# Kernel tuning notes

Measured on AMD Instinct MI355X. Metric: run time of the kernel, lower is better.

The kernel has to match this reference:

```python
import jax, jax.numpy as jnp
import numpy as np

H = 4  # heads


def _tconv(x, src, dst, ea, Wq, bq, Wk, bk, Wv, bv, We, Ws, bs):
    # PyG TransformerConv, heads=4, concat=False, root_weight=True, beta=False
    N = x.shape[0]
    Dh = Wq.shape[1] // H  # per-head dim (= hidden_channels)
    q = (x @ Wq + bq).reshape(N, H, Dh)
    k = (x @ Wk + bk).reshape(N, H, Dh)
    v = (x @ Wv + bv).reshape(N, H, Dh)
    e = (ea @ We).reshape(-1, H, Dh)      # lin_edge has no bias in PyG
    kj = k[src] + e                        # [E, H, Dh]
    vj = v[src] + e                        # [E, H, Dh]
    alpha = (q[dst] * kj).sum(-1) / jnp.sqrt(jnp.asarray(Dh, x.dtype))  # [E, H]
    # segment softmax over incoming edges of each dst node
    m = jax.ops.segment_max(alpha, dst, num_segments=N)
    a = jnp.exp(alpha - m[dst])
    s = jax.ops.segment_sum(a, dst, num_segments=N)
    a = a / (s[dst] + 1e-16)
    out = jax.ops.segment_sum(a[:, :, None] * vj, dst, num_segments=N)  # [N, H, Dh]
    out = out.mean(axis=1)                 # concat=False -> mean over heads
    return out + x @ Ws + bs               # root/skip connection


def setup_inputs() -> dict:
    key = jax.random.key(0)
    ks = jax.random.split(key, 32)
    N, E, C_in, C_e, Ch = 50000, 800000, 32, 16, 32
    d = {}
    d['x'] = jax.random.normal(ks[0], (N, C_in), dtype=jnp.float32)
    d['edge_attr'] = jax.random.normal(ks[1], (E, C_e), dtype=jnp.float32)
    d['edge_index'] = jax.random.randint(ks[2], (2, E), 0, N, dtype=jnp.int32)
    s = 0.05
    i = 3
    for L, cin in ((1, C_in), (2, Ch)):
        d[f'Wq{L}'] = jax.random.normal(ks[i], (cin, H * Ch)) * s; i += 1
        d[f'bq{L}'] = jnp.zeros((H * Ch,), jnp.float32)
        d[f'Wk{L}'] = jax.random.normal(ks[i], (cin, H * Ch)) * s; i += 1
        d[f'bk{L}'] = jnp.zeros((H * Ch,), jnp.float32)
        d[f'Wv{L}'] = jax.random.normal(ks[i], (cin, H * Ch)) * s; i += 1
        d[f'bv{L}'] = jnp.zeros((H * Ch,), jnp.float32)
        d[f'We{L}'] = jax.random.normal(ks[i], (C_e, H * Ch)) * s; i += 1
        d[f'Ws{L}'] = jax.random.normal(ks[i], (cin, Ch)) * s; i += 1
        d[f'bs{L}'] = jnp.zeros((Ch,), jnp.float32)
    d['Wm1'] = jax.random.normal(ks[i], (2 * Ch + C_e, Ch)) * s; i += 1
    d['bm1'] = jnp.zeros((Ch,), jnp.float32)
    d['Wm2'] = jax.random.normal(ks[i], (Ch, 1)) * s; i += 1
    d['bm2'] = jnp.zeros((1,), jnp.float32)
    return d


def reference(x, edge_attr, edge_index,
              Wq1, bq1, Wk1, bk1, Wv1, bv1, We1, Ws1, bs1,
              Wq2, bq2, Wk2, bk2, Wv2, bv2, We2, Ws2, bs2,
              Wm1, bm1, Wm2, bm2):
    src, dst = edge_index[0], edge_index[1]
    h = jax.nn.relu(_tconv(x, src, dst, edge_attr, Wq1, bq1, Wk1, bk1, Wv1, bv1, We1, Ws1, bs1))
    h = jax.nn.relu(_tconv(h, src, dst, edge_attr, Wq2, bq2, Wk2, bk2, Wv2, bv2, We2, Ws2, bs2))
    ef = jnp.concatenate([h[src], edge_attr, h[dst]], axis=-1)  # [E, 2*Ch + C_e]
    out = jax.nn.relu(ef @ Wm1 + bm1) @ Wm2 + bm2
    return out.reshape(-1)
```

## Files before the change

kernel.cpp:

```cpp
#include <hip/hip_runtime.h>
#include <math.h>

#define D128 128
#define CH32 32
#define CE16 16

static __device__ __forceinline__ float red32(float t) {
    t += __shfl_xor(t, 1);
    t += __shfl_xor(t, 2);
    t += __shfl_xor(t, 4);
    t += __shfl_xor(t, 8);
    t += __shfl_xor(t, 16);
    return t;
}

__global__ void k_hist(const int* __restrict__ dst, int* __restrict__ deg, int E) {
    int e = blockIdx.x * blockDim.x + threadIdx.x;
    if (e < E) atomicAdd(&deg[dst[e]], 1);
}

__global__ void k_scan1(const int* __restrict__ deg, int* __restrict__ offs,
                        int* __restrict__ bsum, int N) {
    __shared__ int buf[256];
    int t = threadIdx.x;
    int i = blockIdx.x * 256 + t;
    int v = (i < N) ? deg[i] : 0;
    buf[t] = v;
    __syncthreads();
    #pragma unroll
    for (int off = 1; off < 256; off <<= 1) {
        int val = (t >= off) ? buf[t - off] : 0;
        __syncthreads();
        buf[t] += val;
        __syncthreads();
    }
    if (i < N) offs[i] = buf[t] - v;
    if (t == 255) bsum[blockIdx.x] = buf[255];
}

__global__ void k_scan2(const int* __restrict__ bsum, int* __restrict__ boff, int nb) {
    __shared__ int buf[256];
    int t = threadIdx.x;
    int v = (t < nb) ? bsum[t] : 0;
    buf[t] = v;
    __syncthreads();
    #pragma unroll
    for (int off = 1; off < 256; off <<= 1) {
        int val = (t >= off) ? buf[t - off] : 0;
        __syncthreads();
        buf[t] += val;
        __syncthreads();
    }
    if (t < nb) boff[t] = buf[t] - v;
}

__global__ void k_scan3(const int* __restrict__ boff, int* __restrict__ offs,
                        int* __restrict__ cur, int N, int E) {
    int i = blockIdx.x * blockDim.x + threadIdx.x;
    if (i < N) {
        int o = offs[i] + boff[i >> 8];
        offs[i] = o;
        cur[i] = o;
    }
    if (i == 0) offs[N] = E;
}

__global__ void k_scatter(const int* __restrict__ src, const int* __restrict__ dst,
                          int* __restrict__ cur, int* __restrict__ csr_srcb,
                          float4* __restrict__ ea_csr4, const float4* __restrict__ ea4,
                          int E) {
    int e = blockIdx.x * blockDim.x + threadIdx.x;
    if (e < E) {
        int d = dst[e];
        int p = atomicAdd(&cur[d], 1);
        csr_srcb[p] = src[e] << 10;
        float4 a0 = ea4[e * 4 + 0];
        float4 a1 = ea4[e * 4 + 1];
        float4 a2 = ea4[e * 4 + 2];
        float4 a3 = ea4[e * 4 + 3];
        ea_csr4[p * 4 + 0] = a0;
        ea_csr4[p * 4 + 1] = a1;
        ea_csr4[p * 4 + 2] = a2;
        ea_csr4[p * 4 + 3] = a3;
    }
}

__global__ __launch_bounds__(128) void k_nodeproj(
    const float* __restrict__ xin,
    const float* __restrict__ Wq, const float* __restrict__ bq,
    const float* __restrict__ Wk, const float* __restrict__ bk,
    const float* __restrict__ Wv, const float* __restrict__ bv,
    const float* __restrict__ Ws, const float* __restrict__ bs,
    float* __restrict__ q, float* __restrict__ kv,
    float* __restrict__ skip, int N)
{
    int tid = threadIdx.x;
    int c   = tid & 31;
    float wq[32], wk[32], wv[32], ws[32];
    #pragma unroll
    for (int j = 0; j < 32; j++) {
        wq[j] = Wq[j * D128 + tid];
        wk[j] = Wk[j * D128 + tid];
        wv[j] = Wv[j * D128 + tid];
        ws[j] = Ws[j * CH32 + c];
    }
    float bqc = bq[tid], bkc = bk[tid], bvc = bv[tid], bsc = bs[c];
    __shared__ float xs[4][32];
    int nchunk = (N + 3) / 4;
    for (int chk = blockIdx.x; chk < nchunk; chk += gridDim.x) {
        int base = chk * 4;
        {
            int r = tid >> 5;
            int n = base + r;
            xs[r][c] = (n < N) ? xin[n * 32 + c] : 0.f;
        }
        __syncthreads();
        #pragma unroll
        for (int r = 0; r < 4; r++) {
            int n = base + r;
            if (n < N) {
                float aq = bqc, ak = bkc, av = bvc;
                #pragma unroll
                for (int j = 0; j < 32; j++) {
                    float xj = xs[r][j];
                    aq = fmaf(xj, wq[j], aq);
                    ak = fmaf(xj, wk[j], ak);
                    av = fmaf(xj, wv[j], av);
                }
                q[n * D128 + tid] = aq;
                kv[(size_t)n * 256 + tid]       = ak;
                kv[(size_t)n * 256 + 128 + tid] = av;
            }
        }
        {
            int r = tid >> 5;
            int n = base + r;
            if (n < N) {
                float as = bsc;
                #pragma unroll
                for (int j = 0; j < 32; j++) as = fmaf(xs[r][j], ws[j], as);
                skip[n * 32 + c] = as;
            }
        }
        __syncthreads();
    }
}

__global__ __launch_bounds__(128) void k_edgeattn(
    const float* __restrict__ q, const float* __restrict__ kv,
    const float* __restrict__ skip,
    const float* __restrict__ ea_csr, const float* __restrict__ We,
    const int* __restrict__ offs, const int* __restrict__ csr_srcb,
    float* __restrict__ hout)
{
    int node = blockIdx.x;
    int tid = threadIdx.x;
    __shared__ float red[128];

    float we[16];
    #pragma unroll
    for (int j = 0; j < 16; j++) we[j] = We[j * D128 + tid];

    float qv = q[(size_t)node * D128 + tid] * 0.17677669529663687f;
    int s0 = offs[node], s1 = offs[node + 1];

    float l = 0.f, acc = 0.f;
    const char* kvb = (const char*)kv;
    int toff = tid * 4;

    int i = s0;
    if ((s1 - s0) & 1) {
        int sa = csr_srcb[i];
        const char* pa = kvb + (size_t)(unsigned)sa + toff;
        float ka = *(const float*)(pa);
        float va = *(const float*)(pa + 512);
        const float4* ea4 = (const float4*)&ea_csr[(size_t)i * 16];
        float4 a0 = ea4[0], a1 = ea4[1], a2 = ea4[2], a3 = ea4[3];
        float eca;
        eca = a0.x * we[0];
        eca = fmaf(a0.y, we[1],  eca);
        eca = fmaf(a0.z, we[2],  eca);
        eca = fmaf(a0.w, we[3],  eca);
        eca = fmaf(a1.x, we[4],  eca);
        eca = fmaf(a1.y, we[5],  eca);
        eca = fmaf(a1.z, we[6],  eca);
        eca = fmaf(a1.w, we[7],  eca);
        eca = fmaf(a2.x, we[8],  eca);
        eca = fmaf(a2.y, we[9],  eca);
        eca = fmaf(a2.z, we[10], eca);
        eca = fmaf(a2.w, we[11], eca);
        eca = fmaf(a3.x, we[12], eca);
        eca = fmaf(a3.y, we[13], eca);
        eca = fmaf(a3.z, we[14], eca);
        eca = fmaf(a3.w, we[15], eca);
        float alpha = red32(qv * (ka + eca));
        float p = __expf(alpha);
        l += p;
        acc = fmaf(p, va + eca, acc);
        i++;
    }

    for (; i < s1; i += 2) {
        int sa = csr_srcb[i];
        int sb = csr_srcb[i + 1];
        const char* pa = kvb + (size_t)(unsigned)sa + toff;
        const char* pb = kvb + (size_t)(unsigned)sb + toff;
        float ka = *(const float*)(pa);
        float va = *(const float*)(pa + 512);
        float kb = *(const float*)(pb);
        float vb = *(const float*)(pb + 512);
        const float4* ea4 = (const float4*)&ea_csr[(size_t)i * 16];
        float4 a0 = ea4[0], a1 = ea4[1], a2 = ea4[2], a3 = ea4[3];
        float4 b0 = ea4[4], b1 = ea4[5], b2 = ea4[6], b3 = ea4[7];

        float eca, ecb;
        eca = a0.x * we[0];                 ecb = b0.x * we[0];
        eca = fmaf(a0.y, we[1],  eca);      ecb = fmaf(b0.y, we[1],  ecb);
        eca = fmaf(a0.z, we[2],  eca);      ecb = fmaf(b0.z, we[2],  ecb);
        eca = fmaf(a0.w, we[3],  eca);      ecb = fmaf(b0.w, we[3],  ecb);
        eca = fmaf(a1.x, we[4],  eca);      ecb = fmaf(b1.x, we[4],  ecb);
        eca = fmaf(a1.y, we[5],  eca);      ecb = fmaf(b1.y, we[5],  ecb);
        eca = fmaf(a1.z, we[6],  eca);      ecb = fmaf(b1.z, we[6],  ecb);
        eca = fmaf(a1.w, we[7],  eca);      ecb = fmaf(b1.w, we[7],  ecb);
        eca = fmaf(a2.x, we[8],  eca);      ecb = fmaf(b2.x, we[8],  ecb);
        eca = fmaf(a2.y, we[9],  eca);      ecb = fmaf(b2.y, we[9],  ecb);
        eca = fmaf(a2.z, we[10], eca);      ecb = fmaf(b2.z, we[10], ecb);
        eca = fmaf(a2.w, we[11], eca);      ecb = fmaf(b2.w, we[11], ecb);
        eca = fmaf(a3.x, we[12], eca);      ecb = fmaf(b3.x, we[12], ecb);
        eca = fmaf(a3.y, we[13], eca);      ecb = fmaf(b3.y, we[13], ecb);
        eca = fmaf(a3.z, we[14], eca);      ecb = fmaf(b3.z, we[14], ecb);
        eca = fmaf(a3.w, we[15], eca);      ecb = fmaf(b3.w, we[15], ecb);

        float kja = ka + eca, vja = va + eca;
        float kjb = kb + ecb, vjb = vb + ecb;

        float alpha0 = red32(qv * kja);
        float alpha1 = red32(qv * kjb);

        float p0 = __expf(alpha0);
        float p1 = __expf(alpha1);
        l += p0 + p1;
        acc = fmaf(p0, vja, acc);
        acc = fmaf(p1, vjb, acc);
    }

    red[tid] = acc / (l + 1e-16f);
    __syncthreads();
    if (tid < 32) {
        float o = 0.25f * (red[tid] + red[tid + 32] + red[tid + 64] + red[tid + 96])
                + skip[(size_t)node * 32 + tid];
        hout[(size_t)node * 32 + tid] = fmaxf(o, 0.f);
    }
}

__global__ __launch_bounds__(256) void k_mlp(
    const float* __restrict__ h, const float* __restrict__ ea,
    const int* __restrict__ src, const int* __restrict__ dst,
    const float* __restrict__ Wm1, const float* __restrict__ bm1,
    const float* __restrict__ Wm2, const float* __restrict__ bm2,
    float* __restrict__ out, int E)
{
    __shared__ float4 W4[80 * 8];
    __shared__ float bm1L[32];
    __shared__ float wm2L[32];
    int tid = threadIdx.x;
    const float4* Wm1_4 = (const float4*)Wm1;
    for (int i = tid; i < 640; i += 256) W4[i] = Wm1_4[i];
    if (tid < 32) { bm1L[tid] = bm1[tid]; wm2L[tid] = Wm2[tid]; }
    __syncthreads();

    int e = blockIdx.x * 256 + tid;
    if (e >= E) return;
    float b2 = bm2[0];
    int s = src[e], d = dst[e];

    float4 acc[8];
    #pragma unroll
    for (int i = 0; i < 8; i++) acc[i] = make_float4(0.f, 0.f, 0.f, 0.f);

    auto dorow = [&](int j, float xj) {
        #pragma unroll
        for (int c4 = 0; c4 < 8; c4++) {
            float4 w = W4[j * 8 + c4];
            acc[c4].x = fmaf(xj, w.x, acc[c4].x);
            acc[c4].y = fmaf(xj, w.y, acc[c4].y);
            acc[c4].z = fmaf(xj, w.z, acc[c4].z);
            acc[c4].w = fmaf(xj, w.w, acc[c4].w);
        }
    };

    const float4* hs  = (const float4*)(h + (size_t)s * 32);
    const float4* hd  = (const float4*)(h + (size_t)d * 32);
    const float4* eav = (const float4*)(ea + (size_t)e * 16);
    #pragma unroll
    for (int qd = 0; qd < 8; qd++) {
        float4 xv = hs[qd];
        dorow(qd * 4 + 0, xv.x); dorow(qd * 4 + 1, xv.y);
        dorow(qd * 4 + 2, xv.z); dorow(qd * 4 + 3, xv.w);
    }
    #pragma unroll
    for (int qd = 0; qd < 4; qd++) {
        float4 xv = eav[qd];
        dorow(32 + qd * 4 + 0, xv.x); dorow(32 + qd * 4 + 1, xv.y);
        dorow(32 + qd * 4 + 2, xv.z); dorow(32 + qd * 4 + 3, xv.w);
    }
    #pragma unroll
    for (int qd = 0; qd < 8; qd++) {
        float4 xv = hd[qd];
        dorow(48 + qd * 4 + 0, xv.x); dorow(48 + qd * 4 + 1, xv.y);
        dorow(48 + qd * 4 + 2, xv.z); dorow(48 + qd * 4 + 3, xv.w);
    }

    float y = b2;
    #pragma unroll
    for (int c4 = 0; c4 < 8; c4++) {
        y += fmaxf(acc[c4].x + bm1L[c4 * 4 + 0], 0.f) * wm2L[c4 * 4 + 0];
        y += fmaxf(acc[c4].y + bm1L[c4 * 4 + 1], 0.f) * wm2L[c4 * 4 + 1];
        y += fmaxf(acc[c4].z + bm1L[c4 * 4 + 2], 0.f) * wm2L[c4 * 4 + 2];
        y += fmaxf(acc[c4].w + bm1L[c4 * 4 + 3], 0.f) * wm2L[c4 * 4 + 3];
    }
    out[e] = y;
}

extern "C" void kernel_launch(void* const* d_in, const int* in_sizes, int n_in,
                              void* d_out, int out_size, void* d_ws, size_t ws_size,
                              hipStream_t stream)
{
    const float* x  = (const float*)d_in[0];
    const float* ea = (const float*)d_in[1];
    const int*   ei = (const int*)d_in[2];
    const int N = in_sizes[0] / 32;
    const int E = in_sizes[1] / 16;
    const int* src = ei;
    const int* dst = ei + E;

    const float *Wq1 = (const float*)d_in[3],  *bq1 = (const float*)d_in[4];
    const float *Wk1 = (const float*)d_in[5],  *bk1 = (const float*)d_in[6];
    const float *Wv1 = (const float*)d_in[7],  *bv1 = (const float*)d_in[8];
    const float *We1 = (const float*)d_in[9],  *Ws1 = (const float*)d_in[10];
    const float *bs1 = (const float*)d_in[11];
    const float *Wq2 = (const float*)d_in[12], *bq2 = (const float*)d_in[13];
    const float *Wk2 = (const float*)d_in[14], *bk2 = (const float*)d_in[15];
    const float *Wv2 = (const float*)d_in[16], *bv2 = (const float*)d_in[17];
    const float *We2 = (const float*)d_in[18], *Ws2 = (const float*)d_in[19];
    const float *bs2 = (const float*)d_in[20];
    const float *Wm1 = (const float*)d_in[21], *bm1 = (const float*)d_in[22];
    const float *Wm2 = (const float*)d_in[23], *bm2 = (const float*)d_in[24];

    char* w = (char*)d_ws;
    auto alloc = [&](size_t bytes) -> void* {
        void* p = (void*)w;
        w += (bytes + 255) & ~(size_t)255;
        return p;
    };
    int* deg      = (int*)alloc((size_t)N * 4);
    int* offs     = (int*)alloc(((size_t)N + 1) * 4);
    int* cur      = (int*)alloc((size_t)N * 4);
    int* bsum     = (int*)alloc(256 * 4);
    int* boff     = (int*)alloc(256 * 4);
    int* csr_srcb = (int*)alloc((size_t)E * 4);
    float* ea_csr = (float*)alloc((size_t)E * 16 * 4);
    float* qb     = (float*)alloc((size_t)N * 128 * 4);
    float* kvb    = (float*)alloc((size_t)N * 256 * 4);
    float* skipb  = (float*)alloc((size_t)N * 32 * 4);
    float* h1     = (float*)alloc((size_t)N * 32 * 4);
    float* h2     = (float*)alloc((size_t)N * 32 * 4);

    hipMemsetAsync(deg, 0, (size_t)N * 4, stream);

    int ebl = (E + 255) / 256;
    int nb  = (N + 255) / 256;
    k_hist<<<ebl, 256, 0, stream>>>(dst, deg, E);
    k_scan1<<<nb, 256, 0, stream>>>(deg, offs, bsum, N);
    k_scan2<<<1, 256, 0, stream>>>(bsum, boff, nb);
    k_scan3<<<nb, 256, 0, stream>>>(boff, offs, cur, N, E);
    k_scatter<<<ebl, 256, 0, stream>>>(src, dst, cur, csr_srcb,
                                       (float4*)ea_csr, (const float4*)ea, E);

    k_nodeproj<<<1024, 128, 0, stream>>>(x, Wq1, bq1, Wk1, bk1, Wv1, bv1, Ws1, bs1,
                                         qb, kvb, skipb, N);
    k_edgeattn<<<N, 128, 0, stream>>>(qb, kvb, skipb, ea_csr, We1,
                                      offs, csr_srcb, h1);
    k_nodeproj<<<1024, 128, 0, stream>>>(h1, Wq2, bq2, Wk2, bk2, Wv2, bv2, Ws2, bs2,
                                         qb, kvb, skipb, N);
    k_edgeattn<<<N, 128, 0, stream>>>(qb, kvb, skipb, ea_csr, We2,
                                      offs, csr_srcb, h2);
    k_mlp<<<ebl, 256, 0, stream>>>(h2, ea, src, dst, Wm1, bm1, Wm2, bm2,
                                   (float*)d_out, E);
}
```

Before: 606.6 us.

## Factor edge-attribute projection out of per-edge attention loop via q·We precompute

```diff
diff --git a/kernel.cpp b/kernel.cpp
--- a/kernel.cpp
+++ b/kernel.cpp
@@ -154,17 +154,31 @@
     float* __restrict__ hout)
 {
     int node = blockIdx.x;
-    int tid = threadIdx.x;
+    int tid  = threadIdx.x;
+    int head = tid >> 5;
+    int j16  = tid & 15;
     __shared__ float red[128];
 
     float we[16];
     #pragma unroll
-    for (int j = 0; j < 16; j++) we[j] = We[j * D128 + tid];
-
-    float qv = q[(size_t)node * D128 + tid] * 0.17677669529663687f;
+    for (int jj = 0; jj < 16; jj++) we[jj] = We[jj * D128 + tid];
+
+    const float SC = 0.17677669529663687f;
+    float qs = q[(size_t)node * D128 + tid] * SC;
+
+    float wth;
+    {
+        const float* qrow  = &q[(size_t)node * D128 + head * 32];
+        const float* werow = &We[j16 * D128 + head * 32];
+        float s = 0.f;
+        #pragma unroll
+        for (int c = 0; c < 32; c++)
+            s = fmaf(qrow[c], werow[c], s);
+        wth = s * SC * 0.5f;
+    }
+
     int s0 = offs[node], s1 = offs[node + 1];
-
-    float l = 0.f, acc = 0.f;
+    float l = 0.f, accv = 0.f, St = 0.f;
     const char* kvb = (const char*)kv;
     int toff = tid * 4;
 
@@ -172,31 +186,14 @@
     if ((s1 - s0) & 1) {
         int sa = csr_srcb[i];
         const char* pa = kvb + (size_t)(unsigned)sa + toff;
-        float ka = *(const float*)(pa);
-        float va = *(const float*)(pa + 512);
-        const float4* ea4 = (const float4*)&ea_csr[(size_t)i * 16];
-        float4 a0 = ea4[0], a1 = ea4[1], a2 = ea4[2], a3 = ea4[3];
-        float eca;
-        eca = a0.x * we[0];
-        eca = fmaf(a0.y, we[1],  eca);
-        eca = fmaf(a0.z, we[2],  eca);
-        eca = fmaf(a0.w, we[3],  eca);
-        eca = fmaf(a1.x, we[4],  eca);
-        eca = fmaf(a1.y, we[5],  eca);
-        eca = fmaf(a1.z, we[6],  eca);
-        eca = fmaf(a1.w, we[7],  eca);
-        eca = fmaf(a2.x, we[8],  eca);
-        eca = fmaf(a2.y, we[9],  eca);
-        eca = fmaf(a2.z, we[10], eca);
-        eca = fmaf(a2.w, we[11], eca);
-        eca = fmaf(a3.x, we[12], eca);
-        eca = fmaf(a3.y, we[13], eca);
-        eca = fmaf(a3.z, we[14], eca);
-        eca = fmaf(a3.w, we[15], eca);
-        float alpha = red32(qv * (ka + eca));
+        float ka  = *(const float*)(pa);
+        float va  = *(const float*)(pa + 512);
+        float ea0 = ea_csr[(size_t)i * 16 + j16];
+        float alpha = red32(fmaf(qs, ka, ea0 * wth));
         float p = __expf(alpha);
         l += p;
-        acc = fmaf(p, va + eca, acc);
+        accv = fmaf(p, va, accv);
+        St   = fmaf(p, ea0, St);
         i++;
     }
 
@@ -205,46 +202,33 @@
         int sb = csr_srcb[i + 1];
         const char* pa = kvb + (size_t)(unsigned)sa + toff;
         const char* pb = kvb + (size_t)(unsigned)sb + toff;
-        float ka = *(const float*)(pa);
-        float va = *(const float*)(pa + 512);
-        float kb = *(const float*)(pb);
-        float vb = *(const float*)(pb + 512);
-        const float4* ea4 = (const float4*)&ea_csr[(size_t)i * 16];
-        float4 a0 = ea4[0], a1 = ea4[1], a2 = ea4[2], a3 = ea4[3];
-        float4 b0 = ea4[4], b1 = ea4[5], b2 = ea4[6], b3 = ea4[7];
-
-        float eca, ecb;
-        eca = a0.x * we[0];                 ecb = b0.x * we[0];
-        eca = fmaf(a0.y, we[1],  eca);      ecb = fmaf(b0.y, we[1],  ecb);
-        eca = fmaf(a0.z, we[2],  eca);      ecb = fmaf(b0.z, we[2],  ecb);
-        eca = fmaf(a0.w, we[3],  eca);      ecb = fmaf(b0.w, we[3],  ecb);
-        eca = fmaf(a1.x, we[4],  eca);      ecb = fmaf(b1.x, we[4],  ecb);
-        eca = fmaf(a1.y, we[5],  eca);      ecb = fmaf(b1.y, we[5],  ecb);
-        eca = fmaf(a1.z, we[6],  eca);      ecb = fmaf(b1.z, we[6],  ecb);
-        eca = fmaf(a1.w, we[7],  eca);      ecb = fmaf(b1.w, we[7],  ecb);
-        eca = fmaf(a2.x, we[8],  eca);      ecb = fmaf(b2.x, we[8],  ecb);
-        eca = fmaf(a2.y, we[9],  eca);      ecb = fmaf(b2.y, we[9],  ecb);
-        eca = fmaf(a2.z, we[10], eca);      ecb = fmaf(b2.z, we[10], ecb);
-        eca = fmaf(a2.w, we[11], eca);      ecb = fmaf(b2.w, we[11], ecb);
-        eca = fmaf(a3.x, we[12], eca);      ecb = fmaf(b3.x, we[12], ecb);
-        eca = fmaf(a3.y, we[13], eca);      ecb = fmaf(b3.y, we[13], ecb);
-        eca = fmaf(a3.z, we[14], eca);      ecb = fmaf(b3.z, we[14], ecb);
-        eca = fmaf(a3.w, we[15], eca);      ecb = fmaf(b3.w, we[15], ecb);
-
-        float kja = ka + eca, vja = va + eca;
-        float kjb = kb + ecb, vjb = vb + ecb;
-
-        float alpha0 = red32(qv * kja);
-        float alpha1 = red32(qv * kjb);
-
-        float p0 = __expf(alpha0);
-        float p1 = __expf(alpha1);
+        float ka  = *(const float*)(pa);
+        float va  = *(const float*)(pa + 512);
+        float kb  = *(const float*)(pb);
+        float vb  = *(const float*)(pb + 512);
+        float ea0 = ea_csr[(size_t)i * 16 + j16];
+        float ea1 = ea_csr[(size_t)(i + 1) * 16 + j16];
+
+        float a0 = red32(fmaf(qs, ka, ea0 * wth));
+        float a1 = red32(fmaf(qs, kb, ea1 * wth));
+        float p0 = __expf(a0);
+        float p1 = __expf(a1);
         l += p0 + p1;
-        acc = fmaf(p0, vja, acc);
-        acc = fmaf(p1, vjb, acc);
-    }
-
-    red[tid] = acc / (l + 1e-16f);
+        accv = fmaf(p0, va, accv);
+        accv = fmaf(p1, vb, accv);
+        St   = fmaf(p0, ea0, St);
+        St   = fmaf(p1, ea1, St);
+    }
+
+    float acc2 = 0.f;
+    int baselane = (head & 1) * 32;
+    #pragma unroll
+    for (int jj = 0; jj < 16; jj++) {
+        float Sj = __shfl(St, baselane + jj, 64);
+        acc2 = fmaf(we[jj], Sj, acc2);
+    }
+
+    red[tid] = (accv + acc2) / (l + 1e-16f);
     __syncthreads();
     if (tid < 32) {
         float o = 0.25f * (red[tid] + red[tid + 32] + red[tid + 64] + red[tid + 96])
```

Result: slower. 702.7 us (+15.8%).
